# Optimization experiments

Hardware: AMD Instinct MI355X
Metric: run time of the kernel (lower is better)

Reference implementation:

```python
import jax, jax.numpy as jnp
import numpy as np

B, L, E, H, V, NC = 64, 256, 300, 128, 50000, 2
NH1, F1 = 8, 8  # GAT layer 1: 8 heads x 8 features; layer 2: 1 head x 1 feature
LRELU = 0.2


def _lstm_dir(x, W, U, b):
    # x: [B, L, E]; W: [4H, E]; U: [4H, H]; b: [4H] (b_ih + b_hh fused)
    Bq, Hq = x.shape[0], U.shape[1]
    def step(carry, xt):
        h, c = carry
        g = xt @ W.T + h @ U.T + b
        i, f, gg, o = jnp.split(g, 4, axis=-1)  # PyTorch gate order i,f,g,o
        c = jax.nn.sigmoid(f) * c + jax.nn.sigmoid(i) * jnp.tanh(gg)
        h = jax.nn.sigmoid(o) * jnp.tanh(c)
        return (h, c), h
    h0 = jnp.zeros((Bq, Hq), x.dtype)
    _, hs = jax.lax.scan(step, (h0, h0), jnp.swapaxes(x, 0, 1))
    return jnp.swapaxes(hs, 0, 1)  # [B, L, H]


def bilstm(x, Wf, Uf, bf, Wb, Ub, bb):
    hf = _lstm_dir(x, Wf, Uf, bf)
    hb = _lstm_dir(x[:, ::-1], Wb, Ub, bb)[:, ::-1]
    return jnp.concatenate([hf, hb], axis=-1)  # [B, L, 2H]


def gat_layer(x, W, a_src, a_trg, bias, n_heads, f_out, concat, elu_act):
    # Dense equivalent of GAT IMP3 on a fully-connected graph (edge (s,t): src=s, trg=t).
    Bq, Lq, _ = x.shape
    proj = (x @ W.T).reshape(Bq, Lq, n_heads, f_out)        # [B,L,NH,F]
    s_src = jnp.einsum('blhf,hf->blh', proj, a_src)          # [B,L,NH]
    s_trg = jnp.einsum('blhf,hf->blh', proj, a_trg)
    sc = jax.nn.leaky_relu(s_src[:, :, None, :] + s_trg[:, None, :, :], LRELU)  # [B,S,T,NH]
    m = jnp.max(sc, axis=(1, 2, 3), keepdims=True)           # global max per graph (as in IMP3)
    e = jnp.exp(sc - m)
    A = e / (jnp.sum(e, axis=1, keepdims=True) + 1e-16)      # softmax over sources per target
    out = jnp.einsum('bsth,bshf->bthf', A, proj)             # scatter-aggregate to targets
    if concat:
        out = out.reshape(Bq, Lq, n_heads * f_out)
    else:
        out = out.mean(axis=2)
    out = out + bias
    if elu_act:
        out = jax.nn.elu(out)
    return out, A


def setup_inputs() -> dict:
    key = jax.random.key(0)
    ks = jax.random.split(key, 20)
    n = lambda k, shape, s=0.05: (jax.random.normal(k, shape, jnp.float32) * s)
    return {
        'input_ids': jax.random.randint(ks[0], (B, L), 0, V, jnp.int32),
        'attention_mask': jnp.ones((B, L), bool),
        'emb': n(ks[1], (V, E), 0.1),
        'Wih_f': n(ks[2], (4 * H, E)), 'Whh_f': n(ks[3], (4 * H, H)), 'b_f': jnp.zeros((4 * H,), jnp.float32),
        'Wih_b': n(ks[4], (4 * H, E)), 'Whh_b': n(ks[5], (4 * H, H)), 'b_b': jnp.zeros((4 * H,), jnp.float32),
        'g1_W': n(ks[6], (NH1 * F1, 2 * H)), 'g1_src': n(ks[7], (NH1, F1), 0.1), 'g1_trg': n(ks[8], (NH1, F1), 0.1), 'g1_b': jnp.zeros((NH1 * F1,), jnp.float32),
        'g2_W': n(ks[9], (1, NH1 * F1)), 'g2_src': n(ks[10], (1, 1), 0.1), 'g2_trg': n(ks[11], (1, 1), 0.1), 'g2_b': jnp.zeros((1,), jnp.float32),
        'ctx': n(ks[12], (L, 1), 0.1),
        'lin_W': n(ks[13], (B, 2 * H)), 'lin_b': jnp.zeros((B,), jnp.float32),
        'out_W': n(ks[14], (NC, B)), 'out_b': jnp.zeros((NC,), jnp.float32),
    }


def reference(input_ids, attention_mask, emb, Wih_f, Whh_f, b_f, Wih_b, Whh_b, b_b,
              g1_W, g1_src, g1_trg, g1_b, g2_W, g2_src, g2_trg, g2_b,
              ctx, lin_W, lin_b, out_W, out_b):
    x = emb[input_ids]                                   # [B,L,E] (dropout = eval no-op)
    h_seq = bilstm(x, Wih_f, Whh_f, b_f, Wih_b, Whh_b, b_b)  # [B,L,2H]
    h1, _ = gat_layer(h_seq, g1_W, g1_src, g1_trg, g1_b, NH1, F1, True, True)
    _, A2 = gat_layer(h1, g2_W, g2_src, g2_trg, g2_b, 1, 1, False, False)
    att2 = A2[..., 0]                                    # [B, src, trg] == att.view(-1, 2H) rows
    att = jnp.einsum('bst,t->bs', att2, ctx[:, 0])       # mm with context_vector
    att = jnp.where(attention_mask, att, -jnp.inf)
    att = jax.nn.softmax(att, axis=1)                    # [B,L]
    pooled = jnp.max(h_seq * att[..., None], axis=1)     # [B,2H]
    hcl = jax.nn.relu(pooled @ lin_W.T + lin_b)
    logits = hcl @ out_W.T + out_b                       # [B,NC]
    return (logits, att)
```

## Files before the change

kernel.cpp:

```cpp
#include <hip/hip_runtime.h>
#include <math.h>
#include <stdint.h>

#define Bq 64
#define Lq 256
#define Eq 300
#define Hq 128
#define MQ (Bq*Lq)

#define LRELU_S 0.2f

__device__ __forceinline__ float lrelu(float x) { return x > 0.f ? x : LRELU_S * x; }

typedef short short8 __attribute__((ext_vector_type(8)));
typedef float f32x4v __attribute__((ext_vector_type(4)));

__device__ __forceinline__ unsigned short f2bf(float x) {
  unsigned u = __float_as_uint(x);
  u += 0x7FFFu + ((u >> 16) & 1u);
  return (unsigned short)(u >> 16);
}
__device__ __forceinline__ float bf2f(unsigned short h) {
  return __uint_as_float(((unsigned)h) << 16);
}

#define BM 64
#define BN 64
#define BK 16

__global__ __launch_bounds__(256) void gemm_awt(
    const float* __restrict__ Asrc, const int* __restrict__ ids,
    const float* __restrict__ W, const float* __restrict__ bias,
    float* __restrict__ C, int M, int N, int K)
{
  __shared__ float As[BK][BM + 4];
  __shared__ float Bs[BK][BN + 4];
  int tid = threadIdx.x;
  int tx = tid & 15, ty = tid >> 4;
  int row0 = blockIdx.x * BM, col0 = blockIdx.y * BN;

  int lrow = tid >> 2;
  int lk   = (tid & 3) << 2;

  const float* Arow;
  {
    int r = row0 + lrow;
    int id = ids ? ids[r] : r;
    Arow = Asrc + (size_t)id * K;
  }
  const float* Wrow = W + (size_t)(col0 + lrow) * K;

  float acc[4][4] = {};

  for (int k0 = 0; k0 < K; k0 += BK) {
    int kk = k0 + lk;
    float4 av, bv;
    if (kk + 3 < K) {
      av = *(const float4*)(Arow + kk);
      bv = *(const float4*)(Wrow + kk);
    } else {
      float a0 = (kk + 0 < K) ? Arow[kk + 0] : 0.f;
      float a1 = (kk + 1 < K) ? Arow[kk + 1] : 0.f;
      float a2 = (kk + 2 < K) ? Arow[kk + 2] : 0.f;
      float a3 = (kk + 3 < K) ? Arow[kk + 3] : 0.f;
      av = make_float4(a0, a1, a2, a3);
      float b0 = (kk + 0 < K) ? Wrow[kk + 0] : 0.f;
      float b1 = (kk + 1 < K) ? Wrow[kk + 1] : 0.f;
      float b2 = (kk + 2 < K) ? Wrow[kk + 2] : 0.f;
      float b3 = (kk + 3 < K) ? Wrow[kk + 3] : 0.f;
      bv = make_float4(b0, b1, b2, b3);
    }
    As[lk + 0][lrow] = av.x; As[lk + 1][lrow] = av.y;
    As[lk + 2][lrow] = av.z; As[lk + 3][lrow] = av.w;
    Bs[lk + 0][lrow] = bv.x; Bs[lk + 1][lrow] = bv.y;
    Bs[lk + 2][lrow] = bv.z; Bs[lk + 3][lrow] = bv.w;
    __syncthreads();

    #pragma unroll
    for (int k = 0; k < BK; ++k) {
      float4 a4 = *(const float4*)&As[k][ty * 4];
      float4 b4 = *(const float4*)&Bs[k][tx * 4];
      float a[4] = {a4.x, a4.y, a4.z, a4.w};
      float bb[4] = {b4.x, b4.y, b4.z, b4.w};
      #pragma unroll
      for (int i = 0; i < 4; ++i)
        #pragma unroll
        for (int j = 0; j < 4; ++j)
          acc[i][j] += a[i] * bb[j];
    }
    __syncthreads();
  }

  #pragma unroll
  for (int i = 0; i < 4; ++i) {
    int r = row0 + ty * 4 + i;
    #pragma unroll
    for (int j = 0; j < 4; ++j) {
      int cidx = col0 + tx * 4 + j;
      float v = acc[i][j] + (bias ? bias[cidx] : 0.f);
      C[(size_t)r * N + cidx] = v;
    }
  }
}

__global__ __launch_bounds__(256) void gemm_gates_mfma(
    const float* __restrict__ emb, const int* __restrict__ ids,
    const float* __restrict__ Wf, const float* __restrict__ bf,
    const float* __restrict__ Wb, const float* __restrict__ bb_,
    float* __restrict__ C)
{
  __shared__ __align__(16) short Ah[128 * 32];
  __shared__ __align__(16) short Al[128 * 32];
  __shared__ __align__(16) short Bh[128 * 32];
  __shared__ __align__(16) short Bl[128 * 32];
  __shared__ int ids_s[128];

  int tid = threadIdx.x;
  int row0 = blockIdx.x * 128;
  int col0 = blockIdx.y * 128;
  const float* W    = (col0 < 512) ? Wf : Wb;
  const float* bias = (col0 < 512) ? bf : bb_;
  int wcol0 = col0 & 511;

  if (tid < 128) ids_s[tid] = ids[row0 + tid];
  __syncthreads();

  int l  = tid & 63, wv = tid >> 6;
  int wm = wv >> 1,  wn = wv & 1;
  int kq = l >> 4,   rl = l & 15;

  f32x4v acc[4][4] = {};

  for (int k0 = 0; k0 < 300; k0 += 32) {
    #pragma unroll
    for (int p = 0; p < 4; ++p) {
      int idx = p * 256 + tid;
      int row = idx >> 3, c4 = idx & 7;
      int gk = k0 + c4 * 4;
      float4 av = make_float4(0.f, 0.f, 0.f, 0.f);
      float4 bv = make_float4(0.f, 0.f, 0.f, 0.f);
      if (gk < 300) {
        av = *(const float4*)(emb + (size_t)ids_s[row] * 300 + gk);
        bv = *(const float4*)(W + (size_t)(wcol0 + row) * 300 + gk);
      }
      int chunk = (c4 >> 1) ^ ((row >> 2) & 3);
      int off = row * 32 + chunk * 8 + (c4 & 1) * 4;
      {
        unsigned short h0 = f2bf(av.x), h1 = f2bf(av.y), h2 = f2bf(av.z), h3 = f2bf(av.w);
        unsigned short l0 = f2bf(av.x - bf2f(h0)), l1 = f2bf(av.y - bf2f(h1));
        unsigned short l2 = f2bf(av.z - bf2f(h2)), l3 = f2bf(av.w - bf2f(h3));
        uint2 ph; ph.x = (unsigned)h0 | ((unsigned)h1 << 16); ph.y = (unsigned)h2 | ((unsigned)h3 << 16);
        uint2 pl; pl.x = (unsigned)l0 | ((unsigned)l1 << 16); pl.y = (unsigned)l2 | ((unsigned)l3 << 16);
        *(uint2*)&Ah[off] = ph;
        *(uint2*)&Al[off] = pl;
      }
      {
        unsigned short h0 = f2bf(bv.x), h1 = f2bf(bv.y), h2 = f2bf(bv.z), h3 = f2bf(bv.w);
        unsigned short l0 = f2bf(bv.x - bf2f(h0)), l1 = f2bf(bv.y - bf2f(h1));
        unsigned short l2 = f2bf(bv.z - bf2f(h2)), l3 = f2bf(bv.w - bf2f(h3));
        uint2 ph; ph.x = (unsigned)h0 | ((unsigned)h1 << 16); ph.y = (unsigned)h2 | ((unsigned)h3 << 16);
        uint2 pl; pl.x = (unsigned)l0 | ((unsigned)l1 << 16); pl.y = (unsigned)l2 | ((unsigned)l3 << 16);
        *(uint2*)&Bh[off] = ph;
        *(uint2*)&Bl[off] = pl;
      }
    }
    __syncthreads();

    short8 ah[4], al_[4], bh[4], bl[4];
    #pragma unroll
    for (int f = 0; f < 4; ++f) {
      int ar = wm * 64 + f * 16 + rl;
      int ac = kq ^ ((ar >> 2) & 3);
      ah[f]  = *(const short8*)&Ah[ar * 32 + ac * 8];
      al_[f] = *(const short8*)&Al[ar * 32 + ac * 8];
      int br = wn * 64 + f * 16 + rl;
      int bc = kq ^ ((br >> 2) & 3);
      bh[f]  = *(const short8*)&Bh[br * 32 + bc * 8];
      bl[f]  = *(const short8*)&Bl[br * 32 + bc * 8];
    }
    #pragma unroll
    for (int fm = 0; fm < 4; ++fm)
      #pragma unroll
      for (int fn = 0; fn < 4; ++fn) {
        acc[fm][fn] = __builtin_amdgcn_mfma_f32_16x16x32_bf16(ah[fm],  bh[fn], acc[fm][fn], 0, 0, 0);
        acc[fm][fn] = __builtin_amdgcn_mfma_f32_16x16x32_bf16(ah[fm],  bl[fn], acc[fm][fn], 0, 0, 0);
        acc[fm][fn] = __builtin_amdgcn_mfma_f32_16x16x32_bf16(al_[fm], bh[fn], acc[fm][fn], 0, 0, 0);
      }
    __syncthreads();
  }

  int fq = l >> 4;
  #pragma unroll
  for (int fm = 0; fm < 4; ++fm) {
    #pragma unroll
    for (int fn = 0; fn < 4; ++fn) {
      int gr = row0 + wm * 64 + fm * 16 + fq * 4;
      int lc = wn * 64 + fn * 16 + rl;
      float bsv = bias[wcol0 + lc];
      #pragma unroll
      for (int i = 0; i < 4; ++i)
        C[(size_t)(gr + i) * 1024 + col0 + lc] = acc[fm][fn][i] + bsv;
    }
  }
}

#define MVB(s0,s1,s2,s3, u0,u1,u2,u3, off) \
  "s_waitcnt lgkmcnt(5)\n" \
  "v_fmac_f32 v88, v" #s0 ", v" #u0 "\n" \
  "v_fmac_f32 v89, v" #s1 ", v" #u1 "\n" \
  "v_fmac_f32 v90, v" #s2 ", v" #u2 "\n" \
  "v_fmac_f32 v91, v" #s3 ", v" #u3 "\n" \
  "ds_read_b128 v[" #s0 ":" #s3 "], v81 offset:" #off "\n"

#define MVT(n, s0,s1,s2,s3, u0,u1,u2,u3) \
  "s_waitcnt lgkmcnt(" #n ")\n" \
  "v_fmac_f32 v88, v" #s0 ", v" #u0 "\n" \
  "v_fmac_f32 v89, v" #s1 ", v" #u1 "\n" \
  "v_fmac_f32 v90, v" #s2 ", v" #u2 "\n" \
  "v_fmac_f32 v91, v" #s3 ", v" #u3 "\n"

#define ULD(lo,hi,off) \
  "global_load_dwordx4 v[" #lo ":" #hi "], v80, %[ub] offset:" #off "\n"

__global__ __launch_bounds__(512, 1) void lstm_kernel(
    const float* __restrict__ ws_base,
    const float* __restrict__ Uf, const float* __restrict__ Ub,
    float* __restrict__ h_seq)
{
  __shared__ __align__(1024) float h_sh[2][Hq];
  int blk = blockIdx.x;
  int b = blk & 63;
  int dir = blk >> 6;
  int j = threadIdx.x;
  int lane = j & 63;
  int w = j >> 6;
  int gate = (lane >> 4) & 3;
  int hidx = (w << 4) | (lane & 15);
  int row = (gate << 7) | hidx;

  const float* U = dir ? Ub : Uf;
  int tt0 = dir ? (Lq - 1) : 0;

  unsigned uo  = (unsigned)row * (Hq * 4u);
  unsigned go0 = (1024u + (unsigned)(b * Lq + tt0) * 1024u
                  + (unsigned)dir * 512u + (unsigned)row) * 4u;
  unsigned ho0 = ((unsigned)(b * Lq + tt0) * 256u
                  + (unsigned)dir * (unsigned)Hq + (unsigned)hidx) * 4u;
  int gd = dir ? -4096 : 4096;
  int hd = dir ? -1024 : 1024;

  unsigned lds_base = (unsigned)(uintptr_t)&h_sh[0][0];
  unsigned ldsr0 = lds_base;
  unsigned ldsw0 = lds_base + 512u + (unsigned)hidx * 4u;

  bool isg = (gate == 2);
  float klog = isg ? -2.8853900817779268f : -1.4426950408889634f;
  float mc = isg ? 2.f : 1.f;
  float ac = isg ? -1.f : 0.f;
  int base4 = (lane & 15) * 4;
  int bp0 = base4, bp1 = base4 + 64, bp2 = base4 + 128, bp3 = base4 + 192;

  if (j < Hq) h_sh[0][j] = 0.f;
  __syncthreads();

  asm volatile(
    "v_mov_b32 v80, %[uo]\n"
    "v_mov_b32 v81, %[ldsr0]\n"
    "v_mov_b32 v82, %[ldsw0]\n"
    "v_mov_b32 v83, %[go0]\n"
    "v_mov_b32 v84, %[ho0]\n"
    "v_mov_b32 v87, 0\n"
    "s_mov_b32 s90, 0\n"
    ULD(128,131,0)   ULD(132,135,16)  ULD(136,139,32)  ULD(140,143,48)
    ULD(144,147,64)  ULD(148,151,80)  ULD(152,155,96)  ULD(156,159,112)
    ULD(160,163,128) ULD(164,167,144) ULD(168,171,160) ULD(172,175,176)
    ULD(176,179,192) ULD(180,183,208) ULD(184,187,224) ULD(188,191,240)
    ULD(192,195,256) ULD(196,199,272) ULD(200,203,288) ULD(204,207,304)
    ULD(208,211,320) ULD(212,215,336) ULD(216,219,352) ULD(220,223,368)
    ULD(224,227,384) ULD(228,231,400) ULD(232,235,416) ULD(236,239,432)
    ULD(240,243,448) ULD(244,247,464) ULD(248,251,480) ULD(252,255,496)
    "global_load_dword v85, v83, %[wsb]\n"
    "s_waitcnt vmcnt(0)\n"
    "Ltop_%=:\n"
    "v_add_u32 v83, %[gd], v83\n"
    "global_load_dword v86, v83, %[wsb]\n"
    "ds_read_b128 v[100:103], v81\n"
    "ds_read_b128 v[104:107], v81 offset:16\n"
    "ds_read_b128 v[108:111], v81 offset:32\n"
    "ds_read_b128 v[112:115], v81 offset:48\n"
    "ds_read_b128 v[116:119], v81 offset:64\n"
    "ds_read_b128 v[120:123], v81 offset:80\n"
    "v_mov_b32 v88, v85\n"
    "v_mov_b32 v89, 0\n"
    "v_mov_b32 v90, 0\n"
    "v_mov_b32 v91, 0\n"
    MVB(100,101,102,103, 128,129,130,131, 96)
    MVB(104,105,106,107, 132,133,134,135, 112)
    MVB(108,109,110,111, 136,137,138,139, 128)
    MVB(112,113,114,115, 140,141,142,143, 144)
    MVB(116,117,118,119, 144,145,146,147, 160)
    MVB(120,121,122,123, 148,149,150,151, 176)
    MVB(100,101,102,103, 152,153,154,155, 192)
    MVB(104,105,106,107, 156,157,158,159, 208)
    MVB(108,109,110,111, 160,161,162,163, 224)
    MVB(112,113,114,115, 164,165,166,167, 240)
    MVB(116,117,118,119, 168,169,170,171, 256)
    MVB(120,121,122,123, 172,173,174,175, 272)
    MVB(100,101,102,103, 176,177,178,179, 288)
    MVB(104,105,106,107, 180,181,182,183, 304)
    MVB(108,109,110,111, 184,185,186,187, 320)
    MVB(112,113,114,115, 188,189,190,191, 336)
    MVB(116,117,118,119, 192,193,194,195, 352)
    MVB(120,121,122,123, 196,197,198,199, 368)
    MVB(100,101,102,103, 200,201,202,203, 384)
    MVB(104,105,106,107, 204,205,206,207, 400)
    MVB(108,109,110,111, 208,209,210,211, 416)
    MVB(112,113,114,115, 212,213,214,215, 432)
    MVB(116,117,118,119, 216,217,218,219, 448)
    MVB(120,121,122,123, 220,221,222,223, 464)
    MVB(100,101,102,103, 224,225,226,227, 480)
    MVB(104,105,106,107, 228,229,230,231, 496)
    MVT(5, 108,109,110,111, 232,233,234,235)
    MVT(4, 112,113,114,115, 236,237,238,239)
    MVT(3, 116,117,118,119, 240,241,242,243)
    MVT(2, 120,121,122,123, 244,245,246,247)
    MVT(1, 100,101,102,103, 248,249,250,251)
    MVT(0, 104,105,106,107, 252,253,254,255)
    "v_add_f32 v88, v88, v90\n"
    "v_add_f32 v89, v89, v91\n"
    "v_add_f32 v88, v88, v89\n"
    "v_mul_f32 v92, %[klog], v88\n"
    "v_exp_f32 v93, v92\n"
    "s_nop 1\n"
    "v_add_f32 v94, 1.0, v93\n"
    "v_rcp_f32 v95, v94\n"
    "s_nop 1\n"
    "v_mul_f32 v96, v94, v95\n"
    "v_sub_f32 v96, 2.0, v96\n"
    "v_mul_f32 v95, v95, v96\n"
    "v_fma_f32 v97, v95, %[mc], %[ac]\n"
    "ds_bpermute_b32 v92, %[bp0], v97\n"
    "ds_bpermute_b32 v93, %[bp1], v97\n"
    "ds_bpermute_b32 v94, %[bp2], v97\n"
    "ds_bpermute_b32 v98, %[bp3], v97\n"
    "s_waitcnt lgkmcnt(0)\n"
    "v_mul_f32 v95, v92, v94\n"
    "v_fma_f32 v87, v93, v87, v95\n"
    "v_mul_f32 v92, 0xc038aa3b, v87\n"
    "v_exp_f32 v93, v92\n"
    "s_nop 1\n"
    "v_add_f32 v94, 1.0, v93\n"
    "v_rcp_f32 v95, v94\n"
    "s_nop 1\n"
    "v_mul_f32 v96, v94, v95\n"
    "v_sub_f32 v96, 2.0, v96\n"
    "v_mul_f32 v95, v95, v96\n"
    "v_fma_f32 v96, v95, 2.0, -1.0\n"
    "v_mul_f32 v96, v98, v96\n"
    "s_waitcnt vmcnt(0)\n"
    "v_mov_b32 v85, v86\n"
    "ds_write_b32 v82, v96\n"
    "global_store_dword v84, v96, %[hsb]\n"
    "v_add_u32 v84, %[hd], v84\n"
    "v_xor_b32 v81, 0x200, v81\n"
    "v_xor_b32 v82, 0x200, v82\n"
    "s_waitcnt lgkmcnt(0)\n"
    "s_barrier\n"
    "s_add_u32 s90, s90, 1\n"
    "s_cmp_lt_u32 s90, 256\n"
    "s_cbranch_scc1 Ltop_%=\n"
    "s_waitcnt vmcnt(0) lgkmcnt(0)\n"
    :
    : [wsb]"s"(ws_base), [hsb]"s"(h_seq), [ub]"s"(U),
      [gd]"s"(gd), [hd]"s"(hd),
      [uo]"v"(uo), [go0]"v"(go0), [ho0]"v"(ho0),
      [ldsr0]"v"(ldsr0), [ldsw0]"v"(ldsw0),
      [klog]"v"(klog), [mc]"v"(mc), [ac]"v"(ac),
      [bp0]"v"(bp0), [bp1]"v"(bp1), [bp2]"v"(bp2), [bp3]"v"(bp3)
    : "memory", "scc", "s90",
      "v80","v81","v82","v83","v84","v85","v86","v87","v88","v89",
      "v90","v91","v92","v93","v94","v95","v96","v97","v98",
      "v100","v101","v102","v103","v104","v105","v106","v107",
      "v108","v109","v110","v111","v112","v113","v114","v115",
      "v116","v117","v118","v119","v120","v121","v122","v123",
      "v128","v129","v130","v131","v132","v133","v134","v135",
      "v136","v137","v138","v139","v140","v141","v142","v143",
      "v144","v145","v146","v147","v148","v149","v150","v151",
      "v152","v153","v154","v155","v156","v157","v158","v159",
      "v160","v161","v162","v163","v164","v165","v166","v167",
      "v168","v169","v170","v171","v172","v173","v174","v175",
      "v176","v177","v178","v179","v180","v181","v182","v183",
      "v184","v185","v186","v187","v188","v189","v190","v191",
      "v192","v193","v194","v195","v196","v197","v198","v199",
      "v200","v201","v202","v203","v204","v205","v206","v207",
      "v208","v209","v210","v211","v212","v213","v214","v215",
      "v216","v217","v218","v219","v220","v221","v222","v223",
      "v224","v225","v226","v227","v228","v229","v230","v231",
      "v232","v233","v234","v235","v236","v237","v238","v239",
      "v240","v241","v242","v243","v244","v245","v246","v247",
      "v248","v249","v250","v251","v252","v253","v254","v255");
}
#undef MVB
#undef MVT
#undef ULD

__device__ __forceinline__ float block_max_256(float v, volatile float* red) {
  #pragma unroll
  for (int o = 32; o > 0; o >>= 1) v = fmaxf(v, __shfl_xor(v, o, 64));
  int tid = threadIdx.x;
  if ((tid & 63) == 0) red[tid >> 6] = v;
  __syncthreads();
  float r = fmaxf(fmaxf(red[0], red[1]), fmaxf(red[2], red[3]));
  __syncthreads();
  return r;
}
__device__ __forceinline__ float block_sum_256(float v, volatile float* red) {
  #pragma unroll
  for (int o = 32; o > 0; o >>= 1) v += __shfl_xor(v, o, 64);
  int tid = threadIdx.x;
  if ((tid & 63) == 0) red[tid >> 6] = v;
  __syncthreads();
  float r = red[0] + red[1] + red[2] + red[3];
  __syncthreads();
  return r;
}

__global__ __launch_bounds__(256) void gat1_fused_kernel(
    const float* __restrict__ proj1, const float* __restrict__ g1_src,
    const float* __restrict__ g1_trg, const float* __restrict__ g1_b,
    float* __restrict__ h1)
{
  int b = blockIdx.x >> 3;
  int h = blockIdx.x & 7;
  int t = threadIdx.x;
  __shared__ float src_s[Lq], trg_s[Lq];
  __shared__ float proj_s[Lq * 8];
  __shared__ float red[4];

  size_t base = (size_t)b * Lq;
  float pv[8];
  {
    const float4* pr = (const float4*)(proj1 + (base + t) * 64 + h * 8);
    float4 p0 = pr[0], p1 = pr[1];
    pv[0]=p0.x; pv[1]=p0.y; pv[2]=p0.z; pv[3]=p0.w;
    pv[4]=p1.x; pv[5]=p1.y; pv[6]=p1.z; pv[7]=p1.w;
    float4* psh = (float4*)(proj_s + t * 8);
    psh[0] = p0; psh[1] = p1;
  }
  float ss = 0.f, st = 0.f;
  #pragma unroll
  for (int f = 0; f < 8; ++f) {
    ss += pv[f] * g1_src[h * 8 + f];
    st += pv[f] * g1_trg[h * 8 + f];
  }
  src_s[t] = ss;
  trg_s[t] = st;
  __syncthreads();

  float ms = block_max_256(ss, red);
  float mt = block_max_256(st, red);
  float m = lrelu(ms + mt);

  float mytrg = trg_s[t];
  float den = 1e-16f;
  float acc[8] = {};
  for (int s = 0; s < Lq; ++s) {
    float wgt = __expf(lrelu(src_s[s] + mytrg) - m);
    den += wgt;
    const float* ps = proj_s + s * 8;
    #pragma unroll
    for (int f = 0; f < 8; ++f) acc[f] += wgt * ps[f];
  }
  float inv = 1.f / den;
  float* out = h1 + (base + t) * 64 + h * 8;
  #pragma unroll
  for (int f = 0; f < 8; ++f) {
    float v = acc[f] * inv + g1_b[h * 8 + f];
    out[f] = v > 0.f ? v : expm1f(v);
  }
}

__global__ __launch_bounds__(256) void gat2_pool_head_kernel(
    const float* __restrict__ h1, const float* __restrict__ g2_W,
    const float* __restrict__ g2_src, const float* __restrict__ g2_trg,
    const float* __restrict__ ctx, const float* __restrict__ h_seq,
    const float* __restrict__ lin_W, const float* __restrict__ lin_b,
    const float* __restrict__ out_W, const float* __restrict__ out_b,
    float* __restrict__ att_out, float* __restrict__ logits)
{
  int b = blockIdx.x;
  int tid = threadIdx.x;
  __shared__ float w2[64];
  __shared__ float src2[Lq], trg2[Lq], dq[Lq], att_sh[Lq], pool_sh[256];
  __shared__ float red[4];
  __shared__ float part[4][64];
  __shared__ float hcl[64];

  if (tid < 64) w2[tid] = g2_W[tid];
  __syncthreads();

  const float* hr = h1 + ((size_t)b * Lq + tid) * 64;
  float p = 0.f;
  #pragma unroll
  for (int k = 0; k < 64; ++k) p += hr[k] * w2[k];
  float a_s = g2_src[0], a_t = g2_trg[0];
  src2[tid] = p * a_s;
  trg2[tid] = p * a_t;
  __syncthreads();

  float ms = block_max_256(src2[tid], red);
  float mt = block_max_256(trg2[tid], red);
  float m2 = lrelu(ms + mt);

  float mytrg = trg2[tid];
  float d0 = 1e-16f, d1 = 0.f, d2 = 0.f, d3 = 0.f;
  for (int s = 0; s < Lq; s += 4) {
    d0 += __expf(lrelu(src2[s + 0] + mytrg) - m2);
    d1 += __expf(lrelu(src2[s + 1] + mytrg) - m2);
    d2 += __expf(lrelu(src2[s + 2] + mytrg) - m2);
    d3 += __expf(lrelu(src2[s + 3] + mytrg) - m2);
  }
  dq[tid] = ctx[tid] / ((d0 + d1) + (d2 + d3));
  __syncthreads();

  float mysrc = src2[tid];
  float r0 = 0.f, r1 = 0.f, r2 = 0.f, r3 = 0.f;
  for (int t = 0; t < Lq; t += 4) {
    r0 += dq[t + 0] * __expf(lrelu(mysrc + trg2[t + 0]) - m2);
    r1 += dq[t + 1] * __expf(lrelu(mysrc + trg2[t + 1]) - m2);
    r2 += dq[t + 2] * __expf(lrelu(mysrc + trg2[t + 2]) - m2);
    r3 += dq[t + 3] * __expf(lrelu(mysrc + trg2[t + 3]) - m2);
  }
  float raw = (r0 + r1) + (r2 + r3);

  float mr = block_max_256(raw, red);
  float e = __expf(raw - mr);
  float ssum = block_sum_256(e, red);
  float att = e / ssum;
  att_out[(size_t)b * Lq + tid] = att;
  att_sh[tid] = att;
  __syncthreads();

  float pm = -3.4e38f;
  const float* hb = h_seq + (size_t)b * Lq * 256 + tid;
  for (int l = 0; l < Lq; l += 4) {
    float v0 = hb[(size_t)(l + 0) * 256] * att_sh[l + 0];
    float v1 = hb[(size_t)(l + 1) * 256] * att_sh[l + 1];
    float v2 = hb[(size_t)(l + 2) * 256] * att_sh[l + 2];
    float v3 = hb[(size_t)(l + 3) * 256] * att_sh[l + 3];
    pm = fmaxf(pm, fmaxf(fmaxf(v0, v1), fmaxf(v2, v3)));
  }
  pool_sh[tid] = pm;
  __syncthreads();

  {
    int jj = tid & 63, kq = tid >> 6;
    const float* pr = pool_sh + kq * 64;
    const float* wr = lin_W + jj * 256 + kq * 64;
    float d = 0.f;
    #pragma unroll
    for (int k = 0; k < 64; ++k) d += pr[k] * wr[k];
    part[kq][jj] = d;
  }
  __syncthreads();
  if (tid < 64) {
    float v = part[0][tid] + part[1][tid] + part[2][tid] + part[3][tid] + lin_b[tid];
    hcl[tid] = fmaxf(v, 0.f);
  }
  __syncthreads();
  if (tid < 128) {
    int cc = tid >> 6, jj = tid & 63;
    float pp = hcl[jj] * out_W[cc * 64 + jj];
    #pragma unroll
    for (int o = 32; o > 0; o >>= 1) pp += __shfl_xor(pp, o, 64);
    if (jj == 0) logits[b * 2 + cc] = pp + out_b[cc];
  }
}

extern "C" void kernel_launch(void* const* d_in, const int* in_sizes, int n_in,
                              void* d_out, int out_size, void* d_ws, size_t ws_size,
                              hipStream_t stream)
{
  const int*   ids    = (const int*)  d_in[0];
  const float* emb    = (const float*)d_in[2];
  const float* Wih_f  = (const float*)d_in[3];
  const float* Whh_f  = (const float*)d_in[4];
  const float* b_f    = (const float*)d_in[5];
  const float* Wih_b  = (const float*)d_in[6];
  const float* Whh_b  = (const float*)d_in[7];
  const float* b_b    = (const float*)d_in[8];
  const float* g1_W   = (const float*)d_in[9];
  const float* g1_src = (const float*)d_in[10];
  const float* g1_trg = (const float*)d_in[11];
  const float* g1_b   = (const float*)d_in[12];
  const float* g2_W   = (const float*)d_in[13];
  const float* g2_src = (const float*)d_in[14];
  const float* g2_trg = (const float*)d_in[15];
  const float* ctx    = (const float*)d_in[17];
  const float* lin_W  = (const float*)d_in[18];
  const float* lin_b  = (const float*)d_in[19];
  const float* out_W  = (const float*)d_in[20];
  const float* out_b  = (const float*)d_in[21];

  float* out_f   = (float*)d_out;
  float* logits  = out_f;
  float* att_out = out_f + 128;

  float* ws = (float*)d_ws;
  const size_t M = MQ;
  float* ws_base = ws;
  ws += 1024;
  float* gates   = ws; ws += M * 1024;
  float* h_seq   = ws; ws += M * 256;
  float* proj1   = ws; ws += M * 64;
  float* h1      = ws; ws += M * 64;

  dim3 thr(256);

  gemm_gates_mfma<<<dim3(MQ / 128, 1024 / 128), thr, 0, stream>>>(emb, ids, Wih_f, b_f, Wih_b, b_b, gates);

  lstm_kernel<<<128, 512, 0, stream>>>(ws_base, Whh_f, Whh_b, h_seq);

  gemm_awt<<<dim3(MQ / BM, 1), thr, 0, stream>>>(h_seq, nullptr, g1_W, nullptr, proj1, MQ, 64, 256);
  gat1_fused_kernel<<<Bq * 8, thr, 0, stream>>>(proj1, g1_src, g1_trg, g1_b, h1);

  gat2_pool_head_kernel<<<Bq, thr, 0, stream>>>(h1, g2_W, g2_src, g2_trg, ctx, h_seq,
                                                lin_W, lin_b, out_W, out_b,
                                                att_out, logits);
}
```

Before: 326.1 us.

## Pre-gather and bf16-split embeddings once; drop Newton refinement of rcp in LSTM

Adds a separate kernel that gathers embedding rows and splits them into bf16 hi/lo halves once into a padded buffer. The gates GEMM then loads these pre-split values instead of re-gathering and re-converting the same A rows in each of its 8 column blocks. Separately, the LSTM inline asm drops the Newton-Raphson step after v_rcp_f32 in the sigmoid/tanh, shortening the serial recurrence at some cost in accuracy. The trade is an extra kernel launch and extra workspace traffic.

```diff
diff --git a/kernel.cpp b/kernel.cpp
--- a/kernel.cpp
+++ b/kernel.cpp
@@ -7,6 +7,7 @@
 #define Eq 300
 #define Hq 128
 #define MQ (Bq*Lq)
+#define AST 320
 
 #define LRELU_S 0.2f
 
@@ -22,6 +23,29 @@
 }
 __device__ __forceinline__ float bf2f(unsigned short h) {
   return __uint_as_float(((unsigned)h) << 16);
+}
+
+__global__ __launch_bounds__(256) void gather_conv_kernel(
+    const float* __restrict__ emb, const int* __restrict__ ids,
+    unsigned short* __restrict__ Agh, unsigned short* __restrict__ Agl)
+{
+  const int JOBS = MQ * 80;
+  for (int j = blockIdx.x * blockDim.x + threadIdx.x; j < JOBS;
+       j += gridDim.x * blockDim.x) {
+    int row = j / 80, c = j - row * 80;
+    uint2 ph = make_uint2(0u, 0u), pl = make_uint2(0u, 0u);
+    if (c < 75) {
+      float4 v = *(const float4*)(emb + (size_t)ids[row] * Eq + c * 4);
+      unsigned short h0 = f2bf(v.x), h1 = f2bf(v.y), h2 = f2bf(v.z), h3 = f2bf(v.w);
+      unsigned short l0 = f2bf(v.x - bf2f(h0)), l1 = f2bf(v.y - bf2f(h1));
+      unsigned short l2 = f2bf(v.z - bf2f(h2)), l3 = f2bf(v.w - bf2f(h3));
+      ph.x = (unsigned)h0 | ((unsigned)h1 << 16); ph.y = (unsigned)h2 | ((unsigned)h3 << 16);
+      pl.x = (unsigned)l0 | ((unsigned)l1 << 16); pl.y = (unsigned)l2 | ((unsigned)l3 << 16);
+    }
+    size_t off = (size_t)row * AST + c * 4;
+    *(uint2*)(Agh + off) = ph;
+    *(uint2*)(Agl + off) = pl;
+  }
 }
 
 #define BM 64
@@ -104,7 +128,7 @@
 }
 
 __global__ __launch_bounds__(256) void gemm_gates_mfma(
-    const float* __restrict__ emb, const int* __restrict__ ids,
+    const unsigned short* __restrict__ Agh, const unsigned short* __restrict__ Agl,
     const float* __restrict__ Wf, const float* __restrict__ bf,
     const float* __restrict__ Wb, const float* __restrict__ bb_,
     float* __restrict__ C)
@@ -113,7 +137,6 @@
   __shared__ __align__(16) short Al[128 * 32];
   __shared__ __align__(16) short Bh[128 * 32];
   __shared__ __align__(16) short Bl[128 * 32];
-  __shared__ int ids_s[128];
 
   int tid = threadIdx.x;
   int row0 = blockIdx.x * 128;
@@ -122,9 +145,6 @@
   const float* bias = (col0 < 512) ? bf : bb_;
   int wcol0 = col0 & 511;
 
-  if (tid < 128) ids_s[tid] = ids[row0 + tid];
-  __syncthreads();
-
   int l  = tid & 63, wv = tid >> 6;
   int wm = wv >> 1,  wn = wv & 1;
   int kq = l >> 4,   rl = l & 15;
@@ -137,24 +157,17 @@
       int idx = p * 256 + tid;
       int row = idx >> 3, c4 = idx & 7;
       int gk = k0 + c4 * 4;
-      float4 av = make_float4(0.f, 0.f, 0.f, 0.f);
-      float4 bv = make_float4(0.f, 0.f, 0.f, 0.f);
-      if (gk < 300) {
-        av = *(const float4*)(emb + (size_t)ids_s[row] * 300 + gk);
-        bv = *(const float4*)(W + (size_t)(wcol0 + row) * 300 + gk);
-      }
       int chunk = (c4 >> 1) ^ ((row >> 2) & 3);
       int off = row * 32 + chunk * 8 + (c4 & 1) * 4;
       {
-        unsigned short h0 = f2bf(av.x), h1 = f2bf(av.y), h2 = f2bf(av.z), h3 = f2bf(av.w);
-        unsigned short l0 = f2bf(av.x - bf2f(h0)), l1 = f2bf(av.y - bf2f(h1));
-        unsigned short l2 = f2bf(av.z - bf2f(h2)), l3 = f2bf(av.w - bf2f(h3));
-        uint2 ph; ph.x = (unsigned)h0 | ((unsigned)h1 << 16); ph.y = (unsigned)h2 | ((unsigned)h3 << 16);
-        uint2 pl; pl.x = (unsigned)l0 | ((unsigned)l1 << 16); pl.y = (unsigned)l2 | ((unsigned)l3 << 16);
-        *(uint2*)&Ah[off] = ph;
-        *(uint2*)&Al[off] = pl;
+        size_t ao = (size_t)(row0 + row) * AST + gk;
+        *(uint2*)&Ah[off] = *(const uint2*)(Agh + ao);
+        *(uint2*)&Al[off] = *(const uint2*)(Agl + ao);
       }
       {
+        float4 bv = make_float4(0.f, 0.f, 0.f, 0.f);
+        if (gk < 300)
+          bv = *(const float4*)(W + (size_t)(wcol0 + row) * 300 + gk);
         unsigned short h0 = f2bf(bv.x), h1 = f2bf(bv.y), h2 = f2bf(bv.z), h3 = f2bf(bv.w);
         unsigned short l0 = f2bf(bv.x - bf2f(h0)), l1 = f2bf(bv.y - bf2f(h1));
         unsigned short l2 = f2bf(bv.z - bf2f(h2)), l3 = f2bf(bv.w - bf2f(h3));
@@ -335,9 +348,6 @@
     "v_add_f32 v94, 1.0, v93\n"
     "v_rcp_f32 v95, v94\n"
     "s_nop 1\n"
-    "v_mul_f32 v96, v94, v95\n"
-    "v_sub_f32 v96, 2.0, v96\n"
-    "v_mul_f32 v95, v95, v96\n"
     "v_fma_f32 v97, v95, %[mc], %[ac]\n"
     "ds_bpermute_b32 v92, %[bp0], v97\n"
     "ds_bpermute_b32 v93, %[bp1], v97\n"
@@ -352,9 +362,6 @@
     "v_add_f32 v94, 1.0, v93\n"
     "v_rcp_f32 v95, v94\n"
     "s_nop 1\n"
-    "v_mul_f32 v96, v94, v95\n"
-    "v_sub_f32 v96, 2.0, v96\n"
-    "v_mul_f32 v95, v95, v96\n"
     "v_fma_f32 v96, v95, 2.0, -1.0\n"
     "v_mul_f32 v96, v98, v96\n"
     "s_waitcnt vmcnt(0)\n"
@@ -614,10 +621,14 @@
   float* h_seq   = ws; ws += M * 256;
   float* proj1   = ws; ws += M * 64;
   float* h1      = ws; ws += M * 64;
+  unsigned short* Agh = (unsigned short*)ws; ws += M * AST / 2;
+  unsigned short* Agl = (unsigned short*)ws; ws += M * AST / 2;
 
   dim3 thr(256);
 
-  gemm_gates_mfma<<<dim3(MQ / 128, 1024 / 128), thr, 0, stream>>>(emb, ids, Wih_f, b_f, Wih_b, b_b, gates);
+  gather_conv_kernel<<<2048, thr, 0, stream>>>(emb, ids, Agh, Agl);
+
+  gemm_gates_mfma<<<dim3(MQ / 128, 1024 / 128), thr, 0, stream>>>(Agh, Agl, Wih_f, b_f, Wih_b, b_b, gates);
 
   lstm_kernel<<<128, 512, 0, stream>>>(ws_base, Whh_f, Whh_b, h_seq);
 
```

Result: no change. 328.5 us (+0.7%).
